# Performance work log

Hardware: AMD Instinct MI355X
Metric: run time of the kernel (lower is better)

The kernel has to match this reference:

```python
import jax, jax.numpy as jnp
import numpy as np

D_MODEL = 2048
N_HEADS = 16
N_KV_HEADS = 4
HEAD_DIM = 128
ROPE_THETA = 10000.0


def _rope_cos_sin(T, hd, theta):
    # [T, hd//2]
    inv_freq = 1.0 / (theta ** (jnp.arange(0, hd, 2, dtype=jnp.float32) / hd))
    ang = jnp.arange(T, dtype=jnp.float32)[:, None] * inv_freq[None, :]
    return jnp.cos(ang), jnp.sin(ang)


def _apply_rope(x, cos, sin):
    # x: [B, H, T, hd]; rotate-half (Llama-style) RoPE
    hd = x.shape[-1]
    x1, x2 = x[..., : hd // 2], x[..., hd // 2 :]
    c = cos[None, None, :, :]
    s = sin[None, None, :, :]
    return jnp.concatenate([x1 * c - x2 * s, x2 * c + x1 * s], axis=-1)


def setup_inputs() -> dict:
    key = jax.random.key(0)
    ks = jax.random.split(key, 5)
    B, T = 2, 2048
    x = jax.random.normal(ks[0], (B, T, D_MODEL), dtype=jnp.float32)
    sq = 1.0 / np.sqrt(D_MODEL)
    Wq = jax.random.normal(ks[1], (D_MODEL, N_HEADS * HEAD_DIM), dtype=jnp.float32) * sq
    Wk = jax.random.normal(ks[2], (D_MODEL, N_KV_HEADS * HEAD_DIM), dtype=jnp.float32) * sq
    Wv = jax.random.normal(ks[3], (D_MODEL, N_KV_HEADS * HEAD_DIM), dtype=jnp.float32) * sq
    Wo = jax.random.normal(ks[4], (N_HEADS * HEAD_DIM, D_MODEL), dtype=jnp.float32) * sq
    return {"x": x, "Wq": Wq, "Wk": Wk, "Wv": Wv, "Wo": Wo}


def reference(x, Wq, Wk, Wv, Wo):
    B, T, _ = x.shape
    H, KV, hd = N_HEADS, N_KV_HEADS, HEAD_DIM
    n_rep = H // KV

    q = (x @ Wq).reshape(B, T, H, hd).transpose(0, 2, 1, 3)    # [B,H,T,hd]
    k = (x @ Wk).reshape(B, T, KV, hd).transpose(0, 2, 1, 3)   # [B,KV,T,hd]
    v = (x @ Wv).reshape(B, T, KV, hd).transpose(0, 2, 1, 3)

    cos, sin = _rope_cos_sin(T, hd, ROPE_THETA)
    q = _apply_rope(q, cos, sin)
    k = _apply_rope(k, cos, sin)

    # repeat KV heads for GQA: [B,KV,T,hd] -> [B,H,T,hd]
    k = jnp.repeat(k, n_rep, axis=1)
    v = jnp.repeat(v, n_rep, axis=1)

    scale = 1.0 / jnp.sqrt(jnp.float32(hd))
    scores = jnp.einsum("bhqd,bhkd->bhqk", q, k) * scale       # [B,H,T,T]
    causal = jnp.tril(jnp.ones((T, T), dtype=bool))
    scores = jnp.where(causal[None, None, :, :], scores, -jnp.inf)
    attn = jax.nn.softmax(scores, axis=-1)
    out = jnp.einsum("bhqk,bhkd->bhqd", attn, v)               # [B,H,T,hd]
    out = out.transpose(0, 2, 1, 3).reshape(B, T, H * hd)
    return out @ Wo
```

## Files before the change

kernel.cpp:

```cpp
#include <hip/hip_runtime.h>
#include <stdint.h>

#define T_SEQ 2048
#define DM    2048
#define NH    16
#define NKV   4
#define HD    128
#define MROWS 4096
#define NQKV  3072

typedef unsigned short u16;
typedef __bf16 bf16x8 __attribute__((ext_vector_type(8)));
typedef float  f32x4  __attribute__((ext_vector_type(4)));

__device__ __forceinline__ u16 f2b(float f) {
  union { float f; unsigned u; } v; v.f = f;
  return (u16)((v.u + 0x7fffu + ((v.u >> 16) & 1u)) >> 16);
}
__device__ __forceinline__ float b2f(u16 u) {
  union { unsigned u; float f; } v; v.u = ((unsigned)u) << 16;
  return v.f;
}
__device__ __forceinline__ void gl_lds16(const u16* g, u16* l) {
  __builtin_amdgcn_global_load_lds(
      (__attribute__((address_space(1))) void*)g,
      (__attribute__((address_space(3))) void*)l, 16, 0, 0);
}
__device__ __forceinline__ void storev(float* p, float v) { *p = v; }
__device__ __forceinline__ void storev(u16* p, float v)   { *p = f2b(v); }

__global__ __launch_bounds__(256) void k_pre(const float* __restrict__ x,
                                             const float* __restrict__ Wq,
                                             const float* __restrict__ Wk,
                                             const float* __restrict__ Wv,
                                             const float* __restrict__ Wo,
                                             u16* __restrict__ Xb,
                                             u16* __restrict__ WT,
                                             u16* __restrict__ Wot) {
  int bid = blockIdx.x;
  int tid = threadIdx.x;
  if (bid < 8192) {
    int i = (bid * 256 + tid) * 4;
    float4 v = *(const float4*)(x + i);
    ushort4 r;
    r.x = f2b(v.x); r.y = f2b(v.y); r.z = f2b(v.z); r.w = f2b(v.w);
    *(ushort4*)(Xb + i) = r;
    return;
  }
  __shared__ float tl[32][33];
  int zz = bid - 8192;
  int z = zz >> 6;
  int ky = zz & 63;
  const float* in; u16* out; int Nd, xt;
  if (z < 64)      { in = Wq; out = WT;               Nd = 2048; xt = z; }
  else if (z < 80) { in = Wk; out = WT + 2048 * 2048; Nd = 512;  xt = z - 64; }
  else if (z < 96) { in = Wv; out = WT + 2560 * 2048; Nd = 512;  xt = z - 80; }
  else             { in = Wo; out = Wot;              Nd = 2048; xt = z - 96; }
  int n0 = xt * 32, k0 = ky * 32;
  int tx = tid & 31, ty = tid >> 5;
#pragma unroll
  for (int i = 0; i < 32; i += 8)
    tl[ty + i][tx] = in[(long)(k0 + ty + i) * Nd + n0 + tx];
  __syncthreads();
#pragma unroll
  for (int i = 0; i < 32; i += 8)
    out[(long)(n0 + ty + i) * 2048 + k0 + tx] = f2b(tl[tx][ty + i]);
}

template <int MODE, typename OutT>
__global__ __launch_bounds__(256) void k_gemm(const u16* __restrict__ A,
                                              const u16* __restrict__ Bt,
                                              OutT* __restrict__ C,
                                              u16* __restrict__ Qn,
                                              u16* __restrict__ Kb,
                                              u16* __restrict__ Vc,
                                              int M, int N, int K) {
  __shared__ __align__(16) u16 As[128 * 64];
  __shared__ __align__(16) u16 Bs[128 * 64];
  const int tid = threadIdx.x;
  const int wv = tid >> 6, lane = tid & 63;
  const int quad = lane >> 4, ln = lane & 15;
  const int wm = wv & 1, wn = wv >> 1;
  const int nwg = gridDim.x * gridDim.y;
  const int d = blockIdx.x + blockIdx.y * gridDim.x;
  const int swz = (d & 7) * (nwg >> 3) + (d >> 3);
  const int bx = swz / gridDim.y;
  const int by = swz % gridDim.y;
  const long m0 = (long)bx * 128;
  const long n0 = (long)by * 128;
  f32x4 acc[4][4] = {};
  for (int k0 = 0; k0 < K; k0 += 64) {
#pragma unroll
    for (int r = 0; r < 4; ++r) {
      int c = r * 256 + tid;
      int gc = (c & 7) ^ ((c >> 3) & 7);
      gl_lds16(A  + (m0 + (c >> 3)) * K + k0 + gc * 8, &As[(r * 256 + wv * 64) * 8]);
      gl_lds16(Bt + (n0 + (c >> 3)) * K + k0 + gc * 8, &Bs[(r * 256 + wv * 64) * 8]);
    }
    __syncthreads();
#pragma unroll
    for (int kk = 0; kk < 2; ++kk) {
      const int rs = ((kk << 2) + quad) ^ (ln & 7);
      bf16x8 af[4], bg[4];
#pragma unroll
      for (int i = 0; i < 4; ++i)
        af[i] = *(const bf16x8*)&As[(wm * 64 + i * 16 + ln) * 64 + rs * 8];
#pragma unroll
      for (int j = 0; j < 4; ++j)
        bg[j] = *(const bf16x8*)&Bs[(wn * 32 + (j >> 1) * 64 + (j & 1) * 16 + ln) * 64 + rs * 8];
#pragma unroll
      for (int i = 0; i < 4; ++i)
#pragma unroll
        for (int j = 0; j < 4; ++j)
          acc[i][j] = __builtin_amdgcn_mfma_f32_16x16x32_bf16(af[i], bg[j], acc[i][j], 0, 0, 0);
    }
    __syncthreads();
  }
  if constexpr (MODE == 0) {
#pragma unroll
    for (int i = 0; i < 4; ++i) {
      long row = m0 + wm * 64 + i * 16 + quad * 4;
#pragma unroll
      for (int j = 0; j < 4; ++j) {
        long col = n0 + wn * 32 + (j >> 1) * 64 + (j & 1) * 16 + ln;
#pragma unroll
        for (int r = 0; r < 4; ++r)
          storev(&C[(row + r) * N + col], acc[i][j][r]);
      }
    }
  } else {
    const int nt = by;
    if (nt < 20) {
      const int isQ = nt < 16;
      const int head = isQ ? nt : nt - 16;
      u16* o = isQ ? Qn : Kb;
      const int nh = isQ ? NH : NKV;
      const float qs = isQ ? 0.12751745f : 1.0f;
      const int d0 = wn * 32 + ln;
      const float inv0 = __expf(-0.14391156f * (float)d0);
      const float inv1 = __expf(-0.14391156f * (float)(d0 + 16));
#pragma unroll
      for (int i = 0; i < 4; ++i) {
#pragma unroll
        for (int r = 0; r < 4; ++r) {
          long row = m0 + wm * 64 + i * 16 + quad * 4 + r;
          int b = (int)(row >> 11), t = (int)(row & (T_SEQ - 1));
          long ob = ((long)(b * nh + head) * T_SEQ + t) * HD;
#pragma unroll
          for (int j = 0; j < 2; ++j) {
            int dd = d0 + j * 16;
            float q1 = acc[i][j][r], q2 = acc[i][j + 2][r];
            float sn, cs;
            __sincosf((float)t * (j ? inv1 : inv0), &sn, &cs);
            o[ob + dd]      = f2b((q1 * cs - q2 * sn) * qs);
            o[ob + dd + 64] = f2b((q2 * cs + q1 * sn) * qs);
          }
        }
      }
    } else {
      const int kv = nt - 20;
#pragma unroll
      for (int i = 0; i < 4; ++i) {
#pragma unroll
        for (int r = 0; r < 4; ++r) {
          long row = m0 + wm * 64 + i * 16 + quad * 4 + r;
          int b = (int)(row >> 11), t = (int)(row & (T_SEQ - 1));
          long ob = ((long)(b * NKV + kv) * T_SEQ + t) * HD;
#pragma unroll
          for (int j = 0; j < 4; ++j) {
            int dd = wn * 32 + (j >> 1) * 64 + (j & 1) * 16 + ln;
            Vc[ob + dd] = f2b(acc[i][j][r]);
          }
        }
      }
    }
  }
}

__global__ __launch_bounds__(256) void k_vt(const u16* __restrict__ Vc,
                                            u16* __restrict__ Vt) {
  __shared__ u16 tl[64][68];
  int bkv = blockIdx.z;
  int t0 = blockIdx.x * 64, d0 = blockIdx.y * 64;
  int tx = threadIdx.x & 15, ty = threadIdx.x >> 4;
  const u16* src = Vc + ((long)bkv * T_SEQ + t0) * HD + d0;
#pragma unroll
  for (int ii = 0; ii < 4; ++ii) {
    ushort4 v = *(const ushort4*)&src[(ty + 16 * ii) * HD + tx * 4];
    tl[ty + 16 * ii][tx * 4 + 0] = v.x;
    tl[ty + 16 * ii][tx * 4 + 1] = v.y;
    tl[ty + 16 * ii][tx * 4 + 2] = v.z;
    tl[ty + 16 * ii][tx * 4 + 3] = v.w;
  }
  __syncthreads();
  u16* dst = Vt + ((long)bkv * HD + d0) * T_SEQ + t0;
#pragma unroll
  for (int ii = 0; ii < 4; ++ii) {
    int dr = ty + 16 * ii;
    ushort4 o;
    o.x = tl[tx * 4 + 0][dr];
    o.y = tl[tx * 4 + 1][dr];
    o.z = tl[tx * 4 + 2][dr];
    o.w = tl[tx * 4 + 3][dr];
    *(ushort4*)&dst[(long)dr * T_SEQ + tx * 4] = o;
  }
}

template <bool DIAG>
__device__ __forceinline__ void p_emit(f32x4 (&S)[4], u16* __restrict__ Pb,
                                       int quad, int ln, int mrow) {
#pragma unroll
  for (int nt = 0; nt < 4; ++nt)
#pragma unroll
    for (int r = 0; r < 4; ++r) {
      float v = S[nt][r];
      if (DIAG) v = (nt * 16 + ln <= mrow + r) ? v : -1e30f;
      float pv = exp2f(v - 8.0f);
      int row = quad * 4 + r;
      int chnk = (nt * 2 + (ln >> 3)) ^ (row & 7);
      *(__bf16*)&Pb[row * 64 + chnk * 8 + (ln & 7)] = (__bf16)pv;
    }
}

__global__ __launch_bounds__(256, 2) void k_attn(const u16* __restrict__ Q,
                                                 const u16* __restrict__ Kg,
                                                 const u16* __restrict__ Vt,
                                                 u16* __restrict__ Og) {
  __shared__ __align__(16) u16 Ks[2][64 * 128];
  __shared__ __align__(16) u16 Vs[2][128 * 64];
  __shared__ __align__(16) u16 Ps[4][2][16 * 64];
  const int tid = threadIdx.x;
  const int wv = tid >> 6, lane = tid & 63;
  const int quad = lane >> 4, ln = lane & 15;
  const int bh = blockIdx.y;
  const int b = bh >> 4, h = bh & 15;
  const int kvh = h >> 2;
  const int p = blockIdx.x;
  const int thi = 31 - p, tlo = p;
  const int qhi = thi * 64 + wv * 16;
  const int qlo = tlo * 64 + wv * 16;

  bf16x8 qfh[4], qfl[4];
  {
    const u16* qp = Q + ((long)bh * T_SEQ + qhi + ln) * HD + quad * 8;
#pragma unroll
    for (int s = 0; s < 4; ++s) qfh[s] = *(const bf16x8*)(qp + s * 32);
    qp = Q + ((long)bh * T_SEQ + qlo + ln) * HD + quad * 8;
#pragma unroll
    for (int s = 0; s < 4; ++s) qfl[s] = *(const bf16x8*)(qp + s * 32);
  }
  bf16x8 onesb;
#pragma unroll
  for (int i = 0; i < 8; ++i) onesb[i] = (__bf16)1.0f;

  f32x4 lh = {0.f, 0.f, 0.f, 0.f}, ll = {0.f, 0.f, 0.f, 0.f};
  f32x4 oh[8] = {}, ol[8] = {};

  const u16* Kb = Kg + (long)(b * NKV + kvh) * T_SEQ * HD;
  const u16* Vb = Vt + (long)(b * NKV + kvh) * HD * T_SEQ;

  auto stageKV = [&](int kt, int idx) {
    const int k0 = kt * 64;
#pragma unroll
    for (int r = 0; r < 4; ++r) {
      int s = r * 256 + tid;
      gl_lds16(Kb + (long)(k0 + (s >> 4)) * HD + (((s & 15) ^ ((s >> 4) & 15)) << 3),
               &Ks[idx][(r * 256 + wv * 64) * 8]);
      gl_lds16(Vb + (long)(s >> 3) * T_SEQ + k0 + (((s & 7) ^ ((s >> 3) & 7)) << 3),
               &Vs[idx][(r * 256 + wv * 64) * 8]);
    }
  };

  stageKV(0, 0);
  asm volatile("s_waitcnt vmcnt(0)" ::: "memory");
  __builtin_amdgcn_s_barrier();

  for (int kt = 0; kt <= thi; ++kt) {
    const int cur = kt & 1;
    if (kt < thi) stageKV(kt + 1, cur ^ 1);
    const u16* Ksc = Ks[cur];
    const u16* Vsc = Vs[cur];
    const bool lo_act = (kt <= tlo);
    f32x4 Sh[4], Sl[4];
    __builtin_amdgcn_s_setprio(1);
#pragma unroll
    for (int nt = 0; nt < 4; ++nt) {
      bf16x8 kb[4];
      const u16* kp = &Ksc[(nt * 16 + ln) * 128];
#pragma unroll
      for (int ss = 0; ss < 4; ++ss)
        kb[ss] = *(const bf16x8*)(kp + (((quad + 4 * ss) ^ ln) << 3));
      f32x4 s = {0.f, 0.f, 0.f, 0.f};
#pragma unroll
      for (int ss = 0; ss < 4; ++ss)
        s = __builtin_amdgcn_mfma_f32_16x16x32_bf16(qfh[ss], kb[ss], s, 0, 0, 0);
      Sh[nt] = s;
      if (lo_act) {
        f32x4 t = {0.f, 0.f, 0.f, 0.f};
#pragma unroll
        for (int ss = 0; ss < 4; ++ss)
          t = __builtin_amdgcn_mfma_f32_16x16x32_bf16(qfl[ss], kb[ss], t, 0, 0, 0);
        Sl[nt] = t;
      }
    }
    __builtin_amdgcn_s_setprio(0);
    if (kt == thi) p_emit<true>(Sh, &Ps[wv][0][0], quad, ln, wv * 16 + quad * 4);
    else           p_emit<false>(Sh, &Ps[wv][0][0], quad, ln, 0);
    if (lo_act) {
      if (kt == tlo) p_emit<true>(Sl, &Ps[wv][1][0], quad, ln, wv * 16 + quad * 4);
      else           p_emit<false>(Sl, &Ps[wv][1][0], quad, ln, 0);
    }
    asm volatile("s_waitcnt lgkmcnt(0)" ::: "memory");
    bf16x8 pfh[2], pfl[2];
#pragma unroll
    for (int ss = 0; ss < 2; ++ss)
      pfh[ss] = *(const bf16x8*)&Ps[wv][0][ln * 64 + (((ss * 4 + quad) ^ (ln & 7)) << 3)];
    if (lo_act) {
#pragma unroll
      for (int ss = 0; ss < 2; ++ss)
        pfl[ss] = *(const bf16x8*)&Ps[wv][1][ln * 64 + (((ss * 4 + quad) ^ (ln & 7)) << 3)];
    }
    __builtin_amdgcn_s_setprio(1);
    lh = __builtin_amdgcn_mfma_f32_16x16x32_bf16(pfh[0], onesb, lh, 0, 0, 0);
    lh = __builtin_amdgcn_mfma_f32_16x16x32_bf16(pfh[1], onesb, lh, 0, 0, 0);
    if (lo_act) {
      ll = __builtin_amdgcn_mfma_f32_16x16x32_bf16(pfl[0], onesb, ll, 0, 0, 0);
      ll = __builtin_amdgcn_mfma_f32_16x16x32_bf16(pfl[1], onesb, ll, 0, 0, 0);
    }
#pragma unroll
    for (int dt = 0; dt < 8; ++dt) {
      bf16x8 vb[2];
      const u16* vp = &Vsc[(dt * 16 + ln) * 64];
#pragma unroll
      for (int ss = 0; ss < 2; ++ss)
        vb[ss] = *(const bf16x8*)(vp + (((quad + 4 * ss) ^ (ln & 7)) << 3));
#pragma unroll
      for (int ss = 0; ss < 2; ++ss)
        oh[dt] = __builtin_amdgcn_mfma_f32_16x16x32_bf16(pfh[ss], vb[ss], oh[dt], 0, 0, 0);
      if (lo_act) {
#pragma unroll
        for (int ss = 0; ss < 2; ++ss)
          ol[dt] = __builtin_amdgcn_mfma_f32_16x16x32_bf16(pfl[ss], vb[ss], ol[dt], 0, 0, 0);
      }
    }
    __builtin_amdgcn_s_setprio(0);
    asm volatile("s_waitcnt vmcnt(0)" ::: "memory");
    __builtin_amdgcn_s_barrier();
  }
  float rh[4], rl[4];
#pragma unroll
  for (int r = 0; r < 4; ++r) { rh[r] = 1.f / lh[r]; rl[r] = 1.f / ll[r]; }
#pragma unroll
  for (int dt = 0; dt < 8; ++dt)
#pragma unroll
    for (int r = 0; r < 4; ++r) {
      long rowh = (long)b * T_SEQ + qhi + quad * 4 + r;
      long rowl = (long)b * T_SEQ + qlo + quad * 4 + r;
      Og[rowh * (NH * HD) + h * HD + dt * 16 + ln] = f2b(oh[dt][r] * rh[r]);
      Og[rowl * (NH * HD) + h * HD + dt * 16 + ln] = f2b(ol[dt][r] * rl[r]);
    }
}

extern "C" void kernel_launch(void* const* d_in, const int* in_sizes, int n_in,
                              void* d_out, int out_size, void* d_ws, size_t ws_size,
                              hipStream_t stream) {
  const float* x  = (const float*)d_in[0];
  const float* Wq = (const float*)d_in[1];
  const float* Wk = (const float*)d_in[2];
  const float* Wv = (const float*)d_in[3];
  const float* Wo = (const float*)d_in[4];
  float* out = (float*)d_out;
  char* ws = (char*)d_ws;
  u16* WT  = (u16*)(ws + 0);
  u16* Wot = (u16*)(ws + 12582912);
  u16* Vc  = (u16*)(ws + 20971520);
  u16* Qn  = (u16*)(ws + 25165824);
  u16* Xb  = (u16*)(ws + 46137344);
  u16* Kb  = (u16*)(ws + 62914560);
  u16* Vtb = (u16*)(ws + 67108864);
  u16* attn = Xb;

  k_pre<<<18432, 256, 0, stream>>>(x, Wq, Wk, Wv, Wo, Xb, WT, Wot);

  k_gemm<1, u16><<<dim3(32, 24), 256, 0, stream>>>(
      Xb, WT, (u16*)nullptr, Qn, Kb, Vc, MROWS, NQKV, DM);

  k_vt<<<dim3(32, 2, 8), 256, 0, stream>>>(Vc, Vtb);

  k_attn<<<dim3(16, 32), 256, 0, stream>>>(Qn, Kb, Vtb, attn);

  k_gemm<0, float><<<dim3(32, 16), 256, 0, stream>>>(
      attn, Wot, out, nullptr, nullptr, nullptr, MROWS, DM, 2048);
}
```

Baseline: 296.6 us.

## Process four query tiles per attention block to reuse each K/V tile more

The attention kernel now handles four 64-row query tiles per workgroup (two high, two low, causally balanced) instead of two, so each staged K/V tile feeds twice as many MFMA groups. This halves the grid to 256 blocks and cuts K/V global/LDS staging traffic per query row. In exchange it doubles the accumulator register footprint (four sets of O and l), drops launch bounds to one block per CU, and leaves fewer workgroups than a 256-CU part may fill well, with less latency hiding.

```diff
diff --git a/kernel.cpp b/kernel.cpp
--- a/kernel.cpp
+++ b/kernel.cpp
@@ -222,13 +222,13 @@
     }
 }
 
-__global__ __launch_bounds__(256, 2) void k_attn(const u16* __restrict__ Q,
+__global__ __launch_bounds__(256, 1) void k_attn(const u16* __restrict__ Q,
                                                  const u16* __restrict__ Kg,
                                                  const u16* __restrict__ Vt,
                                                  u16* __restrict__ Og) {
   __shared__ __align__(16) u16 Ks[2][64 * 128];
   __shared__ __align__(16) u16 Vs[2][128 * 64];
-  __shared__ __align__(16) u16 Ps[4][2][16 * 64];
+  __shared__ __align__(16) u16 Ps[4][4][16 * 64];
   const int tid = threadIdx.x;
   const int wv = tid >> 6, lane = tid & 63;
   const int quad = lane >> 4, ln = lane & 15;
@@ -236,25 +236,26 @@
   const int b = bh >> 4, h = bh & 15;
   const int kvh = h >> 2;
   const int p = blockIdx.x;
-  const int thi = 31 - p, tlo = p;
-  const int qhi = thi * 64 + wv * 16;
-  const int qlo = tlo * 64 + wv * 16;
-
-  bf16x8 qfh[4], qfl[4];
+  const int t0 = 30 - 2 * p, t1 = 31 - 2 * p;
+  const int t2 = 2 * p,      t3 = 2 * p + 1;
+  const int mrow = wv * 16 + quad * 4;
+
+  bf16x8 qf[4][4];
   {
-    const u16* qp = Q + ((long)bh * T_SEQ + qhi + ln) * HD + quad * 8;
-#pragma unroll
-    for (int s = 0; s < 4; ++s) qfh[s] = *(const bf16x8*)(qp + s * 32);
-    qp = Q + ((long)bh * T_SEQ + qlo + ln) * HD + quad * 8;
-#pragma unroll
-    for (int s = 0; s < 4; ++s) qfl[s] = *(const bf16x8*)(qp + s * 32);
+    const int tq[4] = {t0, t1, t2, t3};
+#pragma unroll
+    for (int st = 0; st < 4; ++st) {
+      const u16* qp = Q + ((long)bh * T_SEQ + tq[st] * 64 + wv * 16 + ln) * HD + quad * 8;
+#pragma unroll
+      for (int s = 0; s < 4; ++s) qf[st][s] = *(const bf16x8*)(qp + s * 32);
+    }
   }
   bf16x8 onesb;
 #pragma unroll
   for (int i = 0; i < 8; ++i) onesb[i] = (__bf16)1.0f;
 
-  f32x4 lh = {0.f, 0.f, 0.f, 0.f}, ll = {0.f, 0.f, 0.f, 0.f};
-  f32x4 oh[8] = {}, ol[8] = {};
+  f32x4 l4[4] = {};
+  f32x4 o[4][8] = {};
 
   const u16* Kb = Kg + (long)(b * NKV + kvh) * T_SEQ * HD;
   const u16* Vb = Vt + (long)(b * NKV + kvh) * HD * T_SEQ;
@@ -275,13 +276,13 @@
   asm volatile("s_waitcnt vmcnt(0)" ::: "memory");
   __builtin_amdgcn_s_barrier();
 
-  for (int kt = 0; kt <= thi; ++kt) {
+  for (int kt = 0; kt <= t1; ++kt) {
     const int cur = kt & 1;
-    if (kt < thi) stageKV(kt + 1, cur ^ 1);
+    if (kt < t1) stageKV(kt + 1, cur ^ 1);
     const u16* Ksc = Ks[cur];
     const u16* Vsc = Vs[cur];
-    const bool lo_act = (kt <= tlo);
-    f32x4 Sh[4], Sl[4];
+    const bool a0 = (kt <= t0), a2 = (kt <= t2), a3 = (kt <= t3);
+    f32x4 S[4][4];
     __builtin_amdgcn_s_setprio(1);
 #pragma unroll
     for (int nt = 0; nt < 4; ++nt) {
@@ -290,42 +291,73 @@
 #pragma unroll
       for (int ss = 0; ss < 4; ++ss)
         kb[ss] = *(const bf16x8*)(kp + (((quad + 4 * ss) ^ ln) << 3));
-      f32x4 s = {0.f, 0.f, 0.f, 0.f};
+      f32x4 s1 = {0.f, 0.f, 0.f, 0.f};
 #pragma unroll
       for (int ss = 0; ss < 4; ++ss)
-        s = __builtin_amdgcn_mfma_f32_16x16x32_bf16(qfh[ss], kb[ss], s, 0, 0, 0);
-      Sh[nt] = s;
-      if (lo_act) {
-        f32x4 t = {0.f, 0.f, 0.f, 0.f};
+        s1 = __builtin_amdgcn_mfma_f32_16x16x32_bf16(qf[1][ss], kb[ss], s1, 0, 0, 0);
+      S[1][nt] = s1;
+      if (a0) {
+        f32x4 z = {0.f, 0.f, 0.f, 0.f};
 #pragma unroll
         for (int ss = 0; ss < 4; ++ss)
-          t = __builtin_amdgcn_mfma_f32_16x16x32_bf16(qfl[ss], kb[ss], t, 0, 0, 0);
-        Sl[nt] = t;
+          z = __builtin_amdgcn_mfma_f32_16x16x32_bf16(qf[0][ss], kb[ss], z, 0, 0, 0);
+        S[0][nt] = z;
+      }
+      if (a2) {
+        f32x4 z = {0.f, 0.f, 0.f, 0.f};
+#pragma unroll
+        for (int ss = 0; ss < 4; ++ss)
+          z = __builtin_amdgcn_mfma_f32_16x16x32_bf16(qf[2][ss], kb[ss], z, 0, 0, 0);
+        S[2][nt] = z;
+      }
+      if (a3) {
+        f32x4 z = {0.f, 0.f, 0.f, 0.f};
+#pragma unroll
+        for (int ss = 0; ss < 4; ++ss)
+          z = __builtin_amdgcn_mfma_f32_16x16x32_bf16(qf[3][ss], kb[ss], z, 0, 0, 0);
+        S[3][nt] = z;
       }
     }
     __builtin_amdgcn_s_setprio(0);
-    if (kt == thi) p_emit<true>(Sh, &Ps[wv][0][0], quad, ln, wv * 16 + quad * 4);
-    else           p_emit<false>(Sh, &Ps[wv][0][0], quad, ln, 0);
-    if (lo_act) {
-      if (kt == tlo) p_emit<true>(Sl, &Ps[wv][1][0], quad, ln, wv * 16 + quad * 4);
-      else           p_emit<false>(Sl, &Ps[wv][1][0], quad, ln, 0);
-    }
+    if (a0) { if (kt == t0) p_emit<true>(S[0], &Ps[wv][0][0], quad, ln, mrow);
+              else          p_emit<false>(S[0], &Ps[wv][0][0], quad, ln, 0); }
+    if (kt == t1) p_emit<true>(S[1], &Ps[wv][1][0], quad, ln, mrow);
+    else          p_emit<false>(S[1], &Ps[wv][1][0], quad, ln, 0);
+    if (a2) { if (kt == t2) p_emit<true>(S[2], &Ps[wv][2][0], quad, ln, mrow);
+              else          p_emit<false>(S[2], &Ps[wv][2][0], quad, ln, 0); }
+    if (a3) { if (kt == t3) p_emit<true>(S[3], &Ps[wv][3][0], quad, ln, mrow);
+              else          p_emit<false>(S[3], &Ps[wv][3][0], quad, ln, 0); }
     asm volatile("s_waitcnt lgkmcnt(0)" ::: "memory");
-    bf16x8 pfh[2], pfl[2];
+    bf16x8 pf[4][2];
 #pragma unroll
     for (int ss = 0; ss < 2; ++ss)
-      pfh[ss] = *(const bf16x8*)&Ps[wv][0][ln * 64 + (((ss * 4 + quad) ^ (ln & 7)) << 3)];
-    if (lo_act) {
+      pf[1][ss] = *(const bf16x8*)&Ps[wv][1][ln * 64 + (((ss * 4 + quad) ^ (ln & 7)) << 3)];
+    if (a0)
 #pragma unroll
       for (int ss = 0; ss < 2; ++ss)
-        pfl[ss] = *(const bf16x8*)&Ps[wv][1][ln * 64 + (((ss * 4 + quad) ^ (ln & 7)) << 3)];
-    }
+        pf[0][ss] = *(const bf16x8*)&Ps[wv][0][ln * 64 + (((ss * 4 + quad) ^ (ln & 7)) << 3)];
+    if (a2)
+#pragma unroll
+      for (int ss = 0; ss < 2; ++ss)
+        pf[2][ss] = *(const bf16x8*)&Ps[wv][2][ln * 64 + (((ss * 4 + quad) ^ (ln & 7)) << 3)];
+    if (a3)
+#pragma unroll
+      for (int ss = 0; ss < 2; ++ss)
+        pf[3][ss] = *(const bf16x8*)&Ps[wv][3][ln * 64 + (((ss * 4 + quad) ^ (ln & 7)) << 3)];
     __builtin_amdgcn_s_setprio(1);
-    lh = __builtin_amdgcn_mfma_f32_16x16x32_bf16(pfh[0], onesb, lh, 0, 0, 0);
-    lh = __builtin_amdgcn_mfma_f32_16x16x32_bf16(pfh[1], onesb, lh, 0, 0, 0);
-    if (lo_act) {
-      ll = __builtin_amdgcn_mfma_f32_16x16x32_bf16(pfl[0], onesb, ll, 0, 0, 0);
-      ll = __builtin_amdgcn_mfma_f32_16x16x32_bf16(pfl[1], onesb, ll, 0, 0, 0);
+    l4[1] = __builtin_amdgcn_mfma_f32_16x16x32_bf16(pf[1][0], onesb, l4[1], 0, 0, 0);
+    l4[1] = __builtin_amdgcn_mfma_f32_16x16x32_bf16(pf[1][1], onesb, l4[1], 0, 0, 0);
+    if (a0) {
+      l4[0] = __builtin_amdgcn_mfma_f32_16x16x32_bf16(pf[0][0], onesb, l4[0], 0, 0, 0);
+      l4[0] = __builtin_amdgcn_mfma_f32_16x16x32_bf16(pf[0][1], onesb, l4[0], 0, 0, 0);
+    }
+    if (a2) {
+      l4[2] = __builtin_amdgcn_mfma_f32_16x16x32_bf16(pf[2][0], onesb, l4[2], 0, 0, 0);
+      l4[2] = __builtin_amdgcn_mfma_f32_16x16x32_bf16(pf[2][1], onesb, l4[2], 0, 0, 0);
+    }
+    if (a3) {
+      l4[3] = __builtin_amdgcn_mfma_f32_16x16x32_bf16(pf[3][0], onesb, l4[3], 0, 0, 0);
+      l4[3] = __builtin_amdgcn_mfma_f32_16x16x32_bf16(pf[3][1], onesb, l4[3], 0, 0, 0);
     }
 #pragma unroll
     for (int dt = 0; dt < 8; ++dt) {
@@ -336,29 +368,40 @@
         vb[ss] = *(const bf16x8*)(vp + (((quad + 4 * ss) ^ (ln & 7)) << 3));
 #pragma unroll
       for (int ss = 0; ss < 2; ++ss)
-        oh[dt] = __builtin_amdgcn_mfma_f32_16x16x32_bf16(pfh[ss], vb[ss], oh[dt], 0, 0, 0);
-      if (lo_act) {
+        o[1][dt] = __builtin_amdgcn_mfma_f32_16x16x32_bf16(pf[1][ss], vb[ss], o[1][dt], 0, 0, 0);
+      if (a0)
 #pragma unroll
         for (int ss = 0; ss < 2; ++ss)
-          ol[dt] = __builtin_amdgcn_mfma_f32_16x16x32_bf16(pfl[ss], vb[ss], ol[dt], 0, 0, 0);
-      }
+          o[0][dt] = __builtin_amdgcn_mfma_f32_16x16x32_bf16(pf[0][ss], vb[ss], o[0][dt], 0, 0, 0);
+      if (a2)
+#pragma unroll
+        for (int ss = 0; ss < 2; ++ss)
+          o[2][dt] = __builtin_amdgcn_mfma_f32_16x16x32_bf16(pf[2][ss], vb[ss], o[2][dt], 0, 0, 0);
+      if (a3)
+#pragma unroll
+        for (int ss = 0; ss < 2; ++ss)
+          o[3][dt] = __builtin_amdgcn_mfma_f32_16x16x32_bf16(pf[3][ss], vb[ss], o[3][dt], 0, 0, 0);
     }
     __builtin_amdgcn_s_setprio(0);
     asm volatile("s_waitcnt vmcnt(0)" ::: "memory");
     __builtin_amdgcn_s_barrier();
   }
-  float rh[4], rl[4];
-#pragma unroll
-  for (int r = 0; r < 4; ++r) { rh[r] = 1.f / lh[r]; rl[r] = 1.f / ll[r]; }
-#pragma unroll
-  for (int dt = 0; dt < 8; ++dt)
-#pragma unroll
-    for (int r = 0; r < 4; ++r) {
-      long rowh = (long)b * T_SEQ + qhi + quad * 4 + r;
-      long rowl = (long)b * T_SEQ + qlo + quad * 4 + r;
-      Og[rowh * (NH * HD) + h * HD + dt * 16 + ln] = f2b(oh[dt][r] * rh[r]);
-      Og[rowl * (NH * HD) + h * HD + dt * 16 + ln] = f2b(ol[dt][r] * rl[r]);
-    }
+  {
+    const int tq[4] = {t0, t1, t2, t3};
+#pragma unroll
+    for (int st = 0; st < 4; ++st) {
+      float rr[4];
+#pragma unroll
+      for (int r = 0; r < 4; ++r) rr[r] = 1.f / l4[st][r];
+#pragma unroll
+      for (int dt = 0; dt < 8; ++dt)
+#pragma unroll
+        for (int r = 0; r < 4; ++r) {
+          long row = (long)b * T_SEQ + tq[st] * 64 + wv * 16 + quad * 4 + r;
+          Og[row * (NH * HD) + h * HD + dt * 16 + ln] = f2b(o[st][dt][r] * rr[r]);
+        }
+    }
+  }
 }
 
 extern "C" void kernel_launch(void* const* d_in, const int* in_sizes, int n_in,
@@ -387,7 +430,7 @@
 
   k_vt<<<dim3(32, 2, 8), 256, 0, stream>>>(Vc, Vtb);
 
-  k_attn<<<dim3(16, 32), 256, 0, stream>>>(Qn, Kb, Vtb, attn);
+  k_attn<<<dim3(8, 32), 256, 0, stream>>>(Qn, Kb, Vtb, attn);
 
   k_gemm<0, float><<<dim3(32, 16), 256, 0, stream>>>(
       attn, Wot, out, nullptr, nullptr, nullptr, MROWS, DM, 2048);
```

After: 336.9 us. +13.6%, slower.
